# Kernel tuning notes

Hardware: AMD Instinct MI355X
Metric: run time of the kernel (lower is better)

Reference implementation:

```python
import jax, jax.numpy as jnp
import numpy as np


def setup_inputs() -> dict:
    key = jax.random.key(0)
    k1, k2, k3 = jax.random.split(key, 3)
    B, L, d = 4, 9, 256
    n_nodes = (B ** L - 1) // (B - 1)  # complete B-ary tree, level order
    vectors = jax.random.normal(k1, (n_nodes, d), dtype=jnp.float32)
    scale = 1.0 / np.sqrt(d)
    Wl = jax.random.normal(k2, (d, d), dtype=jnp.float32) * scale
    Wr = jax.random.normal(k3, (d, d), dtype=jnp.float32) * scale
    return {"vectors": vectors, "Wl": Wl, "Wr": Wr, "branching": B, "n_levels": L}


def reference(vectors, Wl, Wr, branching, n_levels):
    # Complete branching-ary tree stored in level (BFS) order.
    # Leaf: h = vector. Internal: h = tanh(sum_i lc_i*Wl@h_i + rc_i*Wr@h_i + vector)
    B = int(branching)
    L = int(n_levels)
    sizes = [B ** l for l in range(L)]
    offsets = np.concatenate([[0], np.cumsum(sizes)])
    ind = jnp.arange(1, B + 1, dtype=vectors.dtype)
    if B > 1:
        lc = (B - ind) / (B - 1)   # [B]
        rc = (ind - 1) / (B - 1)
    else:
        lc = jnp.full((B,), 0.5, dtype=vectors.dtype)
        rc = jnp.full((B,), 0.5, dtype=vectors.dtype)
    # leaves
    h = vectors[offsets[L - 1]:offsets[L]]  # [B^(L-1), d]
    for l in range(L - 2, -1, -1):
        n_par = sizes[l]
        hl = (h @ Wl.T).reshape(n_par, B, -1)  # [n_par, B, d]
        hr = (h @ Wr.T).reshape(n_par, B, -1)
        contrib = (lc[None, :, None] * hl + rc[None, :, None] * hr).sum(axis=1)
        h = jnp.tanh(contrib + vectors[offsets[l]:offsets[l + 1]])
    return h  # root state, [1, d]
```

## Files before the change

### kernel.cpp

```cpp
#include <hip/hip_runtime.h>
#include <math.h>


typedef __bf16 bf16x8 __attribute__((ext_vector_type(8)));
typedef __bf16 bf16x4 __attribute__((ext_vector_type(4)));
typedef float f32x4 __attribute__((ext_vector_type(4)));

__device__ __forceinline__ float fast_tanh(float x) {
    float ax = fabsf(x);
    float t = __builtin_amdgcn_exp2f(ax * -2.885390082f);
    float r = (1.0f - t) * __builtin_amdgcn_rcpf(1.0f + t);
    return copysignf(r, x);
}

__global__ __launch_bounds__(256) void cbt_wconv(
    const float* __restrict__ Wl, const float* __restrict__ Wr,
    __bf16* __restrict__ Wfrag)
{
    const int t = blockIdx.x * 256 + threadIdx.x;
    const int L = t & 63;
    const int TJ = t >> 6;
    const int T = TJ & 15;
    const int J = TJ >> 4;
    const int n = J * 16 + (L & 15);
    const int k = T * 32 + (L >> 4) * 8;
    const float* src = (k < 256) ? (Wl + (size_t)n * 256 + k)
                                 : (Wr + (size_t)n * 256 + (k - 256));
    const float4 f0 = *reinterpret_cast<const float4*>(src);
    const float4 f1 = *reinterpret_cast<const float4*>(src + 4);
    bf16x8 o;
    o[0] = (__bf16)f0.x; o[1] = (__bf16)f0.y; o[2] = (__bf16)f0.z; o[3] = (__bf16)f0.w;
    o[4] = (__bf16)f1.x; o[5] = (__bf16)f1.y; o[6] = (__bf16)f1.z; o[7] = (__bf16)f1.w;
    *reinterpret_cast<bf16x8*>(Wfrag + (size_t)t * 8) = o;
}

template <int BM, typename CT>
__global__ __launch_bounds__(256, 2) void cbt_mfma(
    const CT* __restrict__ h,
    const __bf16* __restrict__ Wfrag,
    const float* __restrict__ vec,
    __bf16* __restrict__ out,
    int M)
{
    constexpr int MI = BM / 32;
    constexpr int SE = (BM == 64) ? 8 : 4;
    __shared__ __align__(16) __bf16 Alds[BM * 40];

    const int tid = threadIdx.x;
    const int lane = tid & 63;
    const int w = tid >> 6;
    const int wr = w >> 1, wc = w & 1;
    const int mBase = blockIdx.x * BM;
    const int nOff = blockIdx.y * 128;

    f32x4 acc[MI][4] = {};

    const int sm  = (BM == 64) ? (tid >> 2) : (tid >> 3);
    const int skq = (BM == 64) ? ((tid & 3) * 8) : ((tid & 7) * 4);
    const CT* hb = h + (size_t)(mBase + sm) * 1024;

    float ha[SE], hm[SE], hc[SE];
    float cA, cC;
    auto load_h = [&](int k0) {
        const bool isL = (k0 < 256);
        cA = isL ? 1.0f : (1.0f / 3.0f);
        cC = isL ? (1.0f / 3.0f) : 1.0f;
        const CT* base = hb + (isL ? 0 : 256) + (k0 & 255) + skq;
        if constexpr (sizeof(CT) == 4) {
            const float4 a0 = *reinterpret_cast<const float4*>(base);
            const float4 a1 = *reinterpret_cast<const float4*>(base + 4);
            const float4 b0 = *reinterpret_cast<const float4*>(base + 256);
            const float4 b1 = *reinterpret_cast<const float4*>(base + 260);
            const float4 c0 = *reinterpret_cast<const float4*>(base + 512);
            const float4 c1 = *reinterpret_cast<const float4*>(base + 516);
            ha[0]=a0.x; ha[1]=a0.y; ha[2]=a0.z; ha[3]=a0.w;
            ha[4]=a1.x; ha[5]=a1.y; ha[6]=a1.z; ha[7]=a1.w;
            hm[0]=b0.x; hm[1]=b0.y; hm[2]=b0.z; hm[3]=b0.w;
            hm[4]=b1.x; hm[5]=b1.y; hm[6]=b1.z; hm[7]=b1.w;
            hc[0]=c0.x; hc[1]=c0.y; hc[2]=c0.z; hc[3]=c0.w;
            hc[4]=c1.x; hc[5]=c1.y; hc[6]=c1.z; hc[7]=c1.w;
        } else {
            const bf16x4 a = *reinterpret_cast<const bf16x4*>(base);
            const bf16x4 b = *reinterpret_cast<const bf16x4*>(base + 256);
            const bf16x4 c = *reinterpret_cast<const bf16x4*>(base + 512);
#pragma unroll
            for (int j = 0; j < 4; ++j) {
                ha[j] = (float)a[j]; hm[j] = (float)b[j]; hc[j] = (float)c[j];
            }
        }
    };

    auto store_A = [&]() {
        constexpr float CM = 2.0f / 3.0f;
        if constexpr (SE == 8) {
            bf16x8 g;
#pragma unroll
            for (int j = 0; j < 8; ++j)
                g[j] = (__bf16)(cA * ha[j] + CM * hm[j] + cC * hc[j]);
            *reinterpret_cast<bf16x8*>(&Alds[sm * 40 + skq]) = g;
        } else {
            bf16x4 g;
#pragma unroll
            for (int j = 0; j < 4; ++j)
                g[j] = (__bf16)(cA * ha[j] + CM * hm[j] + cC * hc[j]);
            *reinterpret_cast<bf16x4*>(&Alds[sm * 40 + skq]) = g;
        }
    };

    bf16x8 bfr[2][4];
    const size_t J0 = (size_t)(nOff >> 4) + wc * 4;
    auto load_B = [&](int T, int buf) {
        const __bf16* p = Wfrag + ((J0 * 16 + T) * 64 + lane) * 8;
#pragma unroll
        for (int j = 0; j < 4; ++j)
            bfr[buf][j] = *reinterpret_cast<const bf16x8*>(p + (size_t)j * 8192);
    };

    load_h(0);
    load_B(0, 0);

    for (int T = 0; T < 16; ++T) {
        __syncthreads();
        store_A();
        __syncthreads();

        if (T < 15) {
            load_B(T + 1, (T + 1) & 1);
            load_h((T + 1) * 32);
        }

        bf16x8 af[MI];
#pragma unroll
        for (int i = 0; i < MI; ++i)
            af[i] = *reinterpret_cast<const bf16x8*>(
                &Alds[((wr * MI + i) * 16 + (lane & 15)) * 40 + (lane >> 4) * 8]);

#pragma unroll
        for (int i = 0; i < MI; ++i)
#pragma unroll
            for (int j = 0; j < 4; ++j)
                acc[i][j] = __builtin_amdgcn_mfma_f32_16x16x32_bf16(
                    af[i], bfr[T & 1][j], acc[i][j], 0, 0, 0);
    }

    const int q = lane >> 4, n16 = lane & 15;
#pragma unroll
    for (int i = 0; i < MI; ++i) {
        const int mrow = mBase + (wr * MI + i) * 16 + q * 4;
#pragma unroll
        for (int j = 0; j < 4; ++j) {
            const int n = nOff + wc * 64 + j * 16 + n16;
#pragma unroll
            for (int r = 0; r < 4; ++r) {
                const size_t idx = (size_t)(mrow + r) * 256 + n;
                out[idx] = (__bf16)fast_tanh(acc[i][j][r] + vec[idx]);
            }
        }
    }
}

template <typename OT>
__global__ __launch_bounds__(256) void cbt_small(
    const __bf16* __restrict__ h, const float* __restrict__ Wl,
    const float* __restrict__ Wr, const float* __restrict__ vec,
    OT* __restrict__ out)
{
    const int w = blockIdx.x * 4 + (threadIdx.x >> 6);
    const int lane = threadIdx.x & 63;
    const int m = w >> 8;
    const int n = w & 255;

    const __bf16* hbp = h + (size_t)m * 1024 + lane * 4;
    const bf16x4 c0 = *reinterpret_cast<const bf16x4*>(hbp);
    const bf16x4 c1 = *reinterpret_cast<const bf16x4*>(hbp + 256);
    const bf16x4 c2 = *reinterpret_cast<const bf16x4*>(hbp + 512);
    const bf16x4 c3 = *reinterpret_cast<const bf16x4*>(hbp + 768);
    const float4 wl = *reinterpret_cast<const float4*>(Wl + (size_t)n * 256 + lane * 4);
    const float4 wr = *reinterpret_cast<const float4*>(Wr + (size_t)n * 256 + lane * 4);

    constexpr float C23 = 2.0f / 3.0f;
    constexpr float C13 = 1.0f / 3.0f;
    const float wlv[4] = {wl.x, wl.y, wl.z, wl.w};
    const float wrv[4] = {wr.x, wr.y, wr.z, wr.w};
    float acc = 0.0f;
#pragma unroll
    for (int j = 0; j < 4; ++j) {
        const float f0 = (float)c0[j], f1 = (float)c1[j];
        const float f2 = (float)c2[j], f3 = (float)c3[j];
        const float gl = f0 + C23 * f1 + C13 * f2;
        const float gr = C13 * f1 + C23 * f2 + f3;
        acc += gl * wlv[j] + gr * wrv[j];
    }
#pragma unroll
    for (int off = 32; off >= 1; off >>= 1) acc += __shfl_xor(acc, off, 64);

    if (lane == 0)
        out[(size_t)m * 256 + n] = (OT)fast_tanh(acc + vec[(size_t)m * 256 + n]);
}

extern "C" void kernel_launch(void* const* d_in, const int* in_sizes, int n_in,
                              void* d_out, int out_size, void* d_ws, size_t ws_size,
                              hipStream_t stream) {
    const float* vectors = (const float*)d_in[0];
    const float* Wl = (const float*)d_in[1];
    const float* Wr = (const float*)d_in[2];

    __bf16* buf0 = (__bf16*)d_ws;
    __bf16* buf1 = buf0 + (size_t)16384 * 256;
    __bf16* Wfrag = buf1 + (size_t)4096 * 256;

    size_t offsets[10];
    offsets[0] = 0;
    size_t sz = 1;
    for (int l = 0; l < 9; ++l) { offsets[l + 1] = offsets[l] + sz; sz *= 4; }

    hipLaunchKernelGGL(cbt_wconv, dim3(64), dim3(256), 0, stream, Wl, Wr, Wfrag);

    const float* leaf = vectors + offsets[8] * 256;

    hipLaunchKernelGGL((cbt_mfma<64, float>), dim3(256, 2), dim3(256), 0, stream,
                       leaf, Wfrag, vectors + offsets[7] * 256, buf0, 16384);
    hipLaunchKernelGGL((cbt_mfma<32, __bf16>), dim3(128, 2), dim3(256), 0, stream,
                       buf0, Wfrag, vectors + offsets[6] * 256, buf1, 4096);
    hipLaunchKernelGGL((cbt_mfma<32, __bf16>), dim3(32, 2), dim3(256), 0, stream,
                       buf1, Wfrag, vectors + offsets[5] * 256, buf0, 1024);
    hipLaunchKernelGGL((cbt_mfma<32, __bf16>), dim3(8, 2), dim3(256), 0, stream,
                       buf0, Wfrag, vectors + offsets[4] * 256, buf1, 256);
    hipLaunchKernelGGL(cbt_small<__bf16>, dim3(64 * 64), dim3(256), 0, stream,
                       buf1, Wl, Wr, vectors + offsets[3] * 256, buf0);
    hipLaunchKernelGGL(cbt_small<__bf16>, dim3(16 * 64), dim3(256), 0, stream,
                       buf0, Wl, Wr, vectors + offsets[2] * 256, buf1);
    hipLaunchKernelGGL(cbt_small<__bf16>, dim3(4 * 64), dim3(256), 0, stream,
                       buf1, Wl, Wr, vectors + offsets[1] * 256, buf0);
    hipLaunchKernelGGL(cbt_small<float>, dim3(1 * 64), dim3(256), 0, stream,
                       buf0, Wl, Wr, vectors + offsets[0] * 256, (float*)d_out);
}
```

Measured before the change: 187.0 us.

## Use split-bf16 A operand and fp32 intermediates to improve accuracy

The MFMA kernel now splits the aggregated child activations into high and low bf16 parts and runs twice as many MFMAs, so the products are close to fp32 accuracy. Most intermediate level buffers move from bf16 to fp32. Each block now covers all 256 output columns with 32 rows instead of splitting N across two blocks, and the fused left/right aggregation reads all four children once per K step. The main intent looks like a numerical accuracy fix, and it costs extra MFMA work and more memory traffic.

```diff
diff --git a/kernel.cpp b/kernel.cpp
--- a/kernel.cpp
+++ b/kernel.cpp
@@ -34,168 +34,170 @@
     *reinterpret_cast<bf16x8*>(Wfrag + (size_t)t * 8) = o;
 }
 
-template <int BM, typename CT>
+template <typename CT, typename OT>
 __global__ __launch_bounds__(256, 2) void cbt_mfma(
     const CT* __restrict__ h,
     const __bf16* __restrict__ Wfrag,
     const float* __restrict__ vec,
-    __bf16* __restrict__ out,
-    int M)
+    OT* __restrict__ out)
 {
-    constexpr int MI = BM / 32;
-    constexpr int SE = (BM == 64) ? 8 : 4;
-    __shared__ __align__(16) __bf16 Alds[BM * 40];
+    __shared__ __align__(16) __bf16 Alds[4 * 32 * 40];
 
     const int tid = threadIdx.x;
     const int lane = tid & 63;
     const int w = tid >> 6;
     const int wr = w >> 1, wc = w & 1;
-    const int mBase = blockIdx.x * BM;
-    const int nOff = blockIdx.y * 128;
-
-    f32x4 acc[MI][4] = {};
-
-    const int sm  = (BM == 64) ? (tid >> 2) : (tid >> 3);
-    const int skq = (BM == 64) ? ((tid & 3) * 8) : ((tid & 7) * 4);
-    const CT* hb = h + (size_t)(mBase + sm) * 1024;
-
-    float ha[SE], hm[SE], hc[SE];
-    float cA, cC;
+    const int mBase = blockIdx.x * 32;
+
+    f32x4 acc[8] = {};
+
+    const int sm  = tid >> 3;
+    const int skq = (tid & 7) * 4;
+    const CT* hb = h + (size_t)(mBase + sm) * 1024 + skq;
+
+    float c0[4], c1[4], c2[4], c3[4];
     auto load_h = [&](int k0) {
-        const bool isL = (k0 < 256);
-        cA = isL ? 1.0f : (1.0f / 3.0f);
-        cC = isL ? (1.0f / 3.0f) : 1.0f;
-        const CT* base = hb + (isL ? 0 : 256) + (k0 & 255) + skq;
         if constexpr (sizeof(CT) == 4) {
-            const float4 a0 = *reinterpret_cast<const float4*>(base);
-            const float4 a1 = *reinterpret_cast<const float4*>(base + 4);
-            const float4 b0 = *reinterpret_cast<const float4*>(base + 256);
-            const float4 b1 = *reinterpret_cast<const float4*>(base + 260);
-            const float4 c0 = *reinterpret_cast<const float4*>(base + 512);
-            const float4 c1 = *reinterpret_cast<const float4*>(base + 516);
-            ha[0]=a0.x; ha[1]=a0.y; ha[2]=a0.z; ha[3]=a0.w;
-            ha[4]=a1.x; ha[5]=a1.y; ha[6]=a1.z; ha[7]=a1.w;
-            hm[0]=b0.x; hm[1]=b0.y; hm[2]=b0.z; hm[3]=b0.w;
-            hm[4]=b1.x; hm[5]=b1.y; hm[6]=b1.z; hm[7]=b1.w;
-            hc[0]=c0.x; hc[1]=c0.y; hc[2]=c0.z; hc[3]=c0.w;
-            hc[4]=c1.x; hc[5]=c1.y; hc[6]=c1.z; hc[7]=c1.w;
+            const float4 a = *reinterpret_cast<const float4*>(hb + k0);
+            const float4 b = *reinterpret_cast<const float4*>(hb + k0 + 256);
+            const float4 c = *reinterpret_cast<const float4*>(hb + k0 + 512);
+            const float4 d = *reinterpret_cast<const float4*>(hb + k0 + 768);
+            c0[0] = a.x; c0[1] = a.y; c0[2] = a.z; c0[3] = a.w;
+            c1[0] = b.x; c1[1] = b.y; c1[2] = b.z; c1[3] = b.w;
+            c2[0] = c.x; c2[1] = c.y; c2[2] = c.z; c2[3] = c.w;
+            c3[0] = d.x; c3[1] = d.y; c3[2] = d.z; c3[3] = d.w;
         } else {
-            const bf16x4 a = *reinterpret_cast<const bf16x4*>(base);
-            const bf16x4 b = *reinterpret_cast<const bf16x4*>(base + 256);
-            const bf16x4 c = *reinterpret_cast<const bf16x4*>(base + 512);
+            const bf16x4 a = *reinterpret_cast<const bf16x4*>(hb + k0);
+            const bf16x4 b = *reinterpret_cast<const bf16x4*>(hb + k0 + 256);
+            const bf16x4 c = *reinterpret_cast<const bf16x4*>(hb + k0 + 512);
+            const bf16x4 d = *reinterpret_cast<const bf16x4*>(hb + k0 + 768);
 #pragma unroll
             for (int j = 0; j < 4; ++j) {
-                ha[j] = (float)a[j]; hm[j] = (float)b[j]; hc[j] = (float)c[j];
+                c0[j] = (float)a[j]; c1[j] = (float)b[j];
+                c2[j] = (float)c[j]; c3[j] = (float)d[j];
             }
         }
     };
 
     auto store_A = [&]() {
-        constexpr float CM = 2.0f / 3.0f;
-        if constexpr (SE == 8) {
-            bf16x8 g;
-#pragma unroll
-            for (int j = 0; j < 8; ++j)
-                g[j] = (__bf16)(cA * ha[j] + CM * hm[j] + cC * hc[j]);
-            *reinterpret_cast<bf16x8*>(&Alds[sm * 40 + skq]) = g;
-        } else {
-            bf16x4 g;
-#pragma unroll
-            for (int j = 0; j < 4; ++j)
-                g[j] = (__bf16)(cA * ha[j] + CM * hm[j] + cC * hc[j]);
-            *reinterpret_cast<bf16x4*>(&Alds[sm * 40 + skq]) = g;
+        constexpr float C23 = 2.0f / 3.0f, C13 = 1.0f / 3.0f;
+        bf16x4 glh, gll, grh, grl;
+#pragma unroll
+        for (int j = 0; j < 4; ++j) {
+            const float gl = c0[j] + C23 * c1[j] + C13 * c2[j];
+            const float gr = C13 * c1[j] + C23 * c2[j] + c3[j];
+            glh[j] = (__bf16)gl;
+            gll[j] = (__bf16)(gl - (float)glh[j]);
+            grh[j] = (__bf16)gr;
+            grl[j] = (__bf16)(gr - (float)grh[j]);
         }
+        const int o = sm * 40 + skq;
+        *reinterpret_cast<bf16x4*>(&Alds[o])        = glh;
+        *reinterpret_cast<bf16x4*>(&Alds[o + 1280]) = gll;
+        *reinterpret_cast<bf16x4*>(&Alds[o + 2560]) = grh;
+        *reinterpret_cast<bf16x4*>(&Alds[o + 3840]) = grl;
     };
 
-    bf16x8 bfr[2][4];
-    const size_t J0 = (size_t)(nOff >> 4) + wc * 4;
-    auto load_B = [&](int T, int buf) {
-        const __bf16* p = Wfrag + ((J0 * 16 + T) * 64 + lane) * 8;
-#pragma unroll
-        for (int j = 0; j < 4; ++j)
+    bf16x8 bfr[2][8];
+    const __bf16* Wb = Wfrag + ((size_t)wc * 128 * 64 + lane) * 8;
+    auto load_B = [&](int s, int buf) {
+        const __bf16* p = Wb + (size_t)s * 512;
+#pragma unroll
+        for (int j = 0; j < 8; ++j)
             bfr[buf][j] = *reinterpret_cast<const bf16x8*>(p + (size_t)j * 8192);
     };
 
     load_h(0);
     load_B(0, 0);
-
-    for (int T = 0; T < 16; ++T) {
+    load_B(8, 1);
+
+    const int arow = (wr * 16 + (lane & 15)) * 40 + (lane >> 4) * 8;
+
+    for (int T = 0; T < 8; ++T) {
         __syncthreads();
         store_A();
         __syncthreads();
 
-        if (T < 15) {
-            load_B(T + 1, (T + 1) & 1);
-            load_h((T + 1) * 32);
-        }
-
-        bf16x8 af[MI];
-#pragma unroll
-        for (int i = 0; i < MI; ++i)
-            af[i] = *reinterpret_cast<const bf16x8*>(
-                &Alds[((wr * MI + i) * 16 + (lane & 15)) * 40 + (lane >> 4) * 8]);
-
-#pragma unroll
-        for (int i = 0; i < MI; ++i)
-#pragma unroll
-            for (int j = 0; j < 4; ++j)
-                acc[i][j] = __builtin_amdgcn_mfma_f32_16x16x32_bf16(
-                    af[i], bfr[T & 1][j], acc[i][j], 0, 0, 0);
+        if (T < 7) load_h((T + 1) * 32);
+
+        const bf16x8 afLh = *reinterpret_cast<const bf16x8*>(&Alds[arow]);
+        const bf16x8 afLl = *reinterpret_cast<const bf16x8*>(&Alds[arow + 1280]);
+#pragma unroll
+        for (int j = 0; j < 8; ++j)
+            acc[j] = __builtin_amdgcn_mfma_f32_16x16x32_bf16(
+                afLh, bfr[0][j], acc[j], 0, 0, 0);
+#pragma unroll
+        for (int j = 0; j < 8; ++j)
+            acc[j] = __builtin_amdgcn_mfma_f32_16x16x32_bf16(
+                afLl, bfr[0][j], acc[j], 0, 0, 0);
+
+        if (T < 7) load_B(T + 1, 0);
+
+        const bf16x8 afRh = *reinterpret_cast<const bf16x8*>(&Alds[arow + 2560]);
+        const bf16x8 afRl = *reinterpret_cast<const bf16x8*>(&Alds[arow + 3840]);
+#pragma unroll
+        for (int j = 0; j < 8; ++j)
+            acc[j] = __builtin_amdgcn_mfma_f32_16x16x32_bf16(
+                afRh, bfr[1][j], acc[j], 0, 0, 0);
+#pragma unroll
+        for (int j = 0; j < 8; ++j)
+            acc[j] = __builtin_amdgcn_mfma_f32_16x16x32_bf16(
+                afRl, bfr[1][j], acc[j], 0, 0, 0);
+
+        if (T < 7) load_B(T + 9, 1);
     }
 
     const int q = lane >> 4, n16 = lane & 15;
-#pragma unroll
-    for (int i = 0; i < MI; ++i) {
-        const int mrow = mBase + (wr * MI + i) * 16 + q * 4;
-#pragma unroll
-        for (int j = 0; j < 4; ++j) {
-            const int n = nOff + wc * 64 + j * 16 + n16;
-#pragma unroll
-            for (int r = 0; r < 4; ++r) {
-                const size_t idx = (size_t)(mrow + r) * 256 + n;
-                out[idx] = (__bf16)fast_tanh(acc[i][j][r] + vec[idx]);
-            }
+    const int mrow = mBase + wr * 16 + q * 4;
+#pragma unroll
+    for (int j = 0; j < 8; ++j) {
+        const int n = wc * 128 + j * 16 + n16;
+#pragma unroll
+        for (int r = 0; r < 4; ++r) {
+            const size_t idx = (size_t)(mrow + r) * 256 + n;
+            out[idx] = (OT)fast_tanh(acc[j][r] + vec[idx]);
         }
     }
 }
 
-template <typename OT>
 __global__ __launch_bounds__(256) void cbt_small(
-    const __bf16* __restrict__ h, const float* __restrict__ Wl,
+    const float* __restrict__ h, const float* __restrict__ Wl,
     const float* __restrict__ Wr, const float* __restrict__ vec,
-    OT* __restrict__ out)
+    float* __restrict__ out)
 {
     const int w = blockIdx.x * 4 + (threadIdx.x >> 6);
     const int lane = threadIdx.x & 63;
     const int m = w >> 8;
     const int n = w & 255;
 
-    const __bf16* hbp = h + (size_t)m * 1024 + lane * 4;
-    const bf16x4 c0 = *reinterpret_cast<const bf16x4*>(hbp);
-    const bf16x4 c1 = *reinterpret_cast<const bf16x4*>(hbp + 256);
-    const bf16x4 c2 = *reinterpret_cast<const bf16x4*>(hbp + 512);
-    const bf16x4 c3 = *reinterpret_cast<const bf16x4*>(hbp + 768);
+    const float* hbp = h + (size_t)m * 1024 + lane * 4;
+    const float4 c0 = *reinterpret_cast<const float4*>(hbp);
+    const float4 c1 = *reinterpret_cast<const float4*>(hbp + 256);
+    const float4 c2 = *reinterpret_cast<const float4*>(hbp + 512);
+    const float4 c3 = *reinterpret_cast<const float4*>(hbp + 768);
     const float4 wl = *reinterpret_cast<const float4*>(Wl + (size_t)n * 256 + lane * 4);
     const float4 wr = *reinterpret_cast<const float4*>(Wr + (size_t)n * 256 + lane * 4);
 
     constexpr float C23 = 2.0f / 3.0f;
     constexpr float C13 = 1.0f / 3.0f;
+    const float f0[4] = {c0.x, c0.y, c0.z, c0.w};
+    const float f1[4] = {c1.x, c1.y, c1.z, c1.w};
+    const float f2[4] = {c2.x, c2.y, c2.z, c2.w};
+    const float f3[4] = {c3.x, c3.y, c3.z, c3.w};
     const float wlv[4] = {wl.x, wl.y, wl.z, wl.w};
     const float wrv[4] = {wr.x, wr.y, wr.z, wr.w};
     float acc = 0.0f;
 #pragma unroll
     for (int j = 0; j < 4; ++j) {
-        const float f0 = (float)c0[j], f1 = (float)c1[j];
-        const float f2 = (float)c2[j], f3 = (float)c3[j];
-        const float gl = f0 + C23 * f1 + C13 * f2;
-        const float gr = C13 * f1 + C23 * f2 + f3;
+        const float gl = f0[j] + C23 * f1[j] + C13 * f2[j];
+        const float gr = C13 * f1[j] + C23 * f2[j] + f3[j];
         acc += gl * wlv[j] + gr * wrv[j];
     }
 #pragma unroll
     for (int off = 32; off >= 1; off >>= 1) acc += __shfl_xor(acc, off, 64);
 
     if (lane == 0)
-        out[(size_t)m * 256 + n] = (OT)fast_tanh(acc + vec[(size_t)m * 256 + n]);
+        out[(size_t)m * 256 + n] = fast_tanh(acc + vec[(size_t)m * 256 + n]);
 }
 
 extern "C" void kernel_launch(void* const* d_in, const int* in_sizes, int n_in,
@@ -205,9 +207,15 @@
     const float* Wl = (const float*)d_in[1];
     const float* Wr = (const float*)d_in[2];
 
-    __bf16* buf0 = (__bf16*)d_ws;
-    __bf16* buf1 = buf0 + (size_t)16384 * 256;
-    __bf16* Wfrag = buf1 + (size_t)4096 * 256;
+    char* p = (char*)d_ws;
+    __bf16* buf7 = (__bf16*)p;           p += (size_t)16384 * 256 * 2;
+    float*  buf6 = (float*)p;            p += (size_t)4096 * 256 * 4;
+    float*  buf5 = (float*)p;            p += (size_t)1024 * 256 * 4;
+    float*  buf4 = (float*)p;            p += (size_t)256 * 256 * 4;
+    float*  buf3 = (float*)p;            p += (size_t)64 * 256 * 4;
+    float*  buf2 = (float*)p;            p += (size_t)16 * 256 * 4;
+    float*  buf1 = (float*)p;            p += (size_t)4 * 256 * 4;
+    __bf16* Wfrag = (__bf16*)p;
 
     size_t offsets[10];
     offsets[0] = 0;
@@ -218,20 +226,20 @@
 
     const float* leaf = vectors + offsets[8] * 256;
 
-    hipLaunchKernelGGL((cbt_mfma<64, float>), dim3(256, 2), dim3(256), 0, stream,
-                       leaf, Wfrag, vectors + offsets[7] * 256, buf0, 16384);
-    hipLaunchKernelGGL((cbt_mfma<32, __bf16>), dim3(128, 2), dim3(256), 0, stream,
-                       buf0, Wfrag, vectors + offsets[6] * 256, buf1, 4096);
-    hipLaunchKernelGGL((cbt_mfma<32, __bf16>), dim3(32, 2), dim3(256), 0, stream,
-                       buf1, Wfrag, vectors + offsets[5] * 256, buf0, 1024);
-    hipLaunchKernelGGL((cbt_mfma<32, __bf16>), dim3(8, 2), dim3(256), 0, stream,
-                       buf0, Wfrag, vectors + offsets[4] * 256, buf1, 256);
-    hipLaunchKernelGGL(cbt_small<__bf16>, dim3(64 * 64), dim3(256), 0, stream,
-                       buf1, Wl, Wr, vectors + offsets[3] * 256, buf0);
-    hipLaunchKernelGGL(cbt_small<__bf16>, dim3(16 * 64), dim3(256), 0, stream,
-                       buf0, Wl, Wr, vectors + offsets[2] * 256, buf1);
-    hipLaunchKernelGGL(cbt_small<__bf16>, dim3(4 * 64), dim3(256), 0, stream,
-                       buf1, Wl, Wr, vectors + offsets[1] * 256, buf0);
-    hipLaunchKernelGGL(cbt_small<float>, dim3(1 * 64), dim3(256), 0, stream,
-                       buf0, Wl, Wr, vectors + offsets[0] * 256, (float*)d_out);
-}
+    hipLaunchKernelGGL((cbt_mfma<float, __bf16>), dim3(512), dim3(256), 0, stream,
+                       leaf, Wfrag, vectors + offsets[7] * 256, buf7);
+    hipLaunchKernelGGL((cbt_mfma<__bf16, float>), dim3(128), dim3(256), 0, stream,
+                       buf7, Wfrag, vectors + offsets[6] * 256, buf6);
+    hipLaunchKernelGGL((cbt_mfma<float, float>), dim3(32), dim3(256), 0, stream,
+                       buf6, Wfrag, vectors + offsets[5] * 256, buf5);
+    hipLaunchKernelGGL((cbt_mfma<float, float>), dim3(8), dim3(256), 0, stream,
+                       buf5, Wfrag, vectors + offsets[4] * 256, buf4);
+    hipLaunchKernelGGL(cbt_small, dim3(64 * 64), dim3(256), 0, stream,
+                       buf4, Wl, Wr, vectors + offsets[3] * 256, buf3);
+    hipLaunchKernelGGL(cbt_small, dim3(16 * 64), dim3(256), 0, stream,
+                       buf3, Wl, Wr, vectors + offsets[2] * 256, buf2);
+    hipLaunchKernelGGL(cbt_small, dim3(4 * 64), dim3(256), 0, stream,
+                       buf2, Wl, Wr, vectors + offsets[1] * 256, buf1);
+    hipLaunchKernelGGL(cbt_small, dim3(1 * 64), dim3(256), 0, stream,
+                       buf1, Wl, Wr, vectors + offsets[0] * 256, (float*)d_out);
+}
```

New measurement: 190.0 us. No clear change (+1.6%).
